# Performance work log

Hardware: AMD Instinct MI355X
Metric: run time of the kernel (lower is better)

Reference implementation:

```python
import jax, jax.numpy as jnp
import numpy as np

B, T = 8, 4096
H, V, K = 512, 32000, 9


def setup_inputs() -> dict:
    key = jax.random.key(0)
    k1, k2, k3 = jax.random.split(key, 3)
    x = jax.random.randint(k1, (B, T), 0, V, dtype=jnp.int32)
    # conv1d weight [out_ch=H, in_ch=V, K], xavier-like scale
    scale = 1.0 / np.sqrt(V * K)
    W = jax.random.normal(k2, (H, V, K), dtype=jnp.float32) * scale
    b = jax.random.normal(k3, (H,), dtype=jnp.float32) * 0.01
    return {"x": x, "W": W, "b": b}


def reference(x, W, b):
    """one_hot(x, V) -> conv1d(V->H, K, pad=K//2) expressed as gather+sum.

    out[b,t,c] = bias[c] + sum_k W[c, x[b, t+k-pad], k]  (zero outside [0,T)).
    """
    Bx, Tx = x.shape
    Hh, Vv, Kk = W.shape
    pad = Kk // 2
    t = jnp.arange(Tx)
    acc = jnp.zeros((Bx, Tx, Hh), dtype=W.dtype)
    for k in range(Kk):  # small fixed kernel loop (K=9)
        src = t + (k - pad)                      # [T]
        valid = (src >= 0) & (src < Tx)          # [T]
        src_c = jnp.clip(src, 0, Tx - 1)
        ids = x[:, src_c]                        # [B,T]
        emb = jnp.take(W[:, :, k].T, ids, axis=0)  # [B,T,H] gather of column k
        acc = acc + jnp.where(valid[None, :, None], emb, jnp.zeros((), W.dtype))
    return acc + b  # [B,T,H]
```

## Files before the change

kernel.cpp:

```cpp
#include <hip/hip_runtime.h>
#include <hip/hip_bf16.h>


#define Hc 512
#define Vc 32000
#define Kc 9
#define Tc 4096
#define Bc 8
#define Mc (Vc * Kc)
#define CHUNK_C 128
#define NCHUNK 4
#define ROW_U (Kc * CHUNK_C / 2)
#define WT_ROWS (Vc + 1)
#define T_TILE 32
#define NTB 9000
#define NGB 1024

__device__ __forceinline__ unsigned short f2bf(float f) {
  unsigned int u = __float_as_uint(f);
  u += 0x7FFFu + ((u >> 16) & 1u);
  return (unsigned short)(u >> 16);
}

__global__ __launch_bounds__(256) void mark_kernel(
    const int* __restrict__ x, int* __restrict__ slot, int* __restrict__ counter) {
  const int i = blockIdx.x * 256 + threadIdx.x;
  const int v = x[i];
  if (atomicCAS(&slot[v], -1, -2147483647) == -1) {
    slot[v] = 1 + atomicAdd(counter, 1);
  }
}

__global__ __launch_bounds__(256) void fused_kernel(
    const float* __restrict__ W, const int* __restrict__ x,
    const int* __restrict__ slot, const float* __restrict__ bias,
    float* __restrict__ out, unsigned int* __restrict__ wbuf,
    const unsigned int* __restrict__ rbuf, int tchunk, int gchunk) {
  __shared__ float tile[64][65];
  const int bx = blockIdx.x;
  const int rem = bx % 10;
  const int tid = threadIdx.x;

  if (rem != 9) {
    if (tchunk >= NCHUNK) return;
    const int tb = (bx / 10) * 9 + rem;
    if (tb >= NTB) return;
    const int mt = tb % 4500;
    const int ct = tb / 4500;
    const int m0 = mt * 64;
    const int cbase = tchunk * CHUNK_C + ct * 64;
    const int tx = tid & 63;
    const int ty = tid >> 6;
#pragma unroll
    for (int r = 0; r < 16; ++r) {
      const int row = ty * 16 + r;
      tile[row][tx] = W[(size_t)(cbase + row) * Mc + (m0 + tx)];
    }
    __syncthreads();
    const int u = tid & 31;
    const int rl = tid >> 5;
#pragma unroll
    for (int p = 0; p < 8; ++p) {
      const int mrow = p * 8 + rl;
      const int m = m0 + mrow;
      const int v = m / Kc;
      const int k = m - v * Kc;
      const int s = slot[v];
      if (s >= 0) {
        const unsigned int val =
            (unsigned int)f2bf(tile[2 * u][mrow]) |
            ((unsigned int)f2bf(tile[2 * u + 1][mrow]) << 16);
        wbuf[(size_t)s * ROW_U + k * (CHUNK_C / 2) + ct * 32 + u] = val;
      }
    }
  } else {
    if (gchunk < 0) return;
    const int gb = bx / 10;
    int* ids = (int*)tile;
    const int b = gb >> 7;
    const int t0 = (gb & 127) * T_TILE;
    if (tid < T_TILE + Kc - 1) {
      const int s = t0 + tid - (Kc / 2);
      ids[tid] = (s >= 0 && s < Tc) ? slot[x[b * Tc + s]] : 0;
    }
    __syncthreads();
    const int lane = tid & 63;
    const int w = tid >> 6;
    const int c0 = gchunk * CHUNK_C;
    const int cpair = c0 + 2 * lane;
    const float2 b2 = *(const float2*)(bias + cpair);
#pragma unroll
    for (int i = 0; i < 8; ++i) {
      const int tt = w * 8 + i;
      float2 acc = b2;
#pragma unroll
      for (int k = 0; k < Kc; ++k) {
        const int id = ids[tt + k];
        const unsigned int wv = rbuf[(size_t)id * ROW_U + k * (CHUNK_C / 2) + lane];
        acc.x += __uint_as_float(wv << 16);
        acc.y += __uint_as_float(wv & 0xFFFF0000u);
      }
      *(float2*)(out + ((size_t)(b * Tc + t0 + tt) << 9) + cpair) = acc;
    }
  }
}

__global__ __launch_bounds__(256) void conv_fallback_kernel(
    const int* __restrict__ x, const float* __restrict__ W,
    const float* __restrict__ bias, float* __restrict__ out) {
  const size_t idx = (size_t)blockIdx.x * 256 + threadIdx.x;
  const int c = (int)(idx & (Hc - 1));
  const size_t bt = idx >> 9;
  const int t = (int)(bt & (Tc - 1));
  const int b = (int)(bt >> 12);
  float acc = bias[c];
#pragma unroll
  for (int k = 0; k < Kc; ++k) {
    const int s = t + k - (Kc / 2);
    if (s >= 0 && s < Tc) {
      const int id = x[b * Tc + s];
      acc += W[(size_t)c * Mc + (size_t)id * Kc + k];
    }
  }
  out[idx] = acc;
}

extern "C" void kernel_launch(void* const* d_in, const int* in_sizes, int n_in,
                              void* d_out, int out_size, void* d_ws, size_t ws_size,
                              hipStream_t stream) {
  const int* x = (const int*)d_in[0];
  const float* W = (const float*)d_in[1];
  const float* bias = (const float*)d_in[2];
  float* out = (float*)d_out;

  const size_t buf_bytes = (size_t)WT_ROWS * ROW_U * 4;
  const size_t buf1_off = buf_bytes;
  const size_t slot_off = 2 * buf_bytes;
  const size_t cnt_off = slot_off + (size_t)Vc * 4;
  const size_t need = cnt_off + 4;

  if (ws_size >= need) {
    unsigned int* buf0 = (unsigned int*)d_ws;
    unsigned int* buf1 = (unsigned int*)((char*)d_ws + buf1_off);
    int* slot = (int*)((char*)d_ws + slot_off);
    int* counter = (int*)((char*)d_ws + cnt_off);
    hipMemsetAsync(slot, 0xFF, (size_t)Vc * 4, stream);
    hipMemsetAsync(counter, 0, 4, stream);
    hipMemsetAsync(buf0, 0, ROW_U * 4, stream);
    hipMemsetAsync(buf1, 0, ROW_U * 4, stream);
    mark_kernel<<<(Bc * Tc) / 256, 256, 0, stream>>>(x, slot, counter);
    const int grid = 10240;
    for (int l = 0; l <= NCHUNK; ++l) {
      const int tchunk = l;
      const int gchunk = l - 1;
      unsigned int* wbuf = (tchunk & 1) ? buf1 : buf0;
      const unsigned int* rbuf = (gchunk >= 0 && (gchunk & 1)) ? buf1 : buf0;
      fused_kernel<<<grid, 256, 0, stream>>>(W, x, slot, bias, out, wbuf, rbuf,
                                             tchunk, gchunk);
    }
  } else {
    const size_t n = (size_t)Bc * Tc * Hc;
    conv_fallback_kernel<<<(int)(n / 256), 256, 0, stream>>>(x, W, bias, out);
  }
}
```

Before: 244.4 us.

## Retile W transpose by vocab groups with swizzled LDS and vectorized bf16 writes

The transpose blocks now cover 7 whole vocab entries (63 m-columns) across all 128 channels of a chunk, where each previously covered 64 m-columns by 64 channels. Tiles go into a swizzled LDS buffer and are written out as uint2 rows per used vocab entry, and a whole vocab row is skipped when it never appears in the input. The grid shrinks to a 4:1 transpose-to-gather block ratio, and W loads and output stores become nontemporal. This aims to cut the per-element slot lookups and scattered 4-byte writes. In exchange, one of 64 lanes sits idle during loads and the per-vocab loop is serial within each block.

```diff
diff --git a/kernel.cpp b/kernel.cpp
--- a/kernel.cpp
+++ b/kernel.cpp
@@ -1,5 +1,6 @@
 #include <hip/hip_runtime.h>
 #include <hip/hip_bf16.h>
+#include <string.h>
 
 
 #define Hc 512
@@ -8,18 +9,21 @@
 #define Tc 4096
 #define Bc 8
 #define Mc (Vc * Kc)
+#define VT 7
+#define NMT 4572
+#define NM_TILE (VT * Kc)
 #define CHUNK_C 128
 #define NCHUNK 4
 #define ROW_U (Kc * CHUNK_C / 2)
 #define WT_ROWS (Vc + 1)
 #define T_TILE 32
-#define NTB 9000
 #define NGB 1024
+#define GRID_N 5715
 
-__device__ __forceinline__ unsigned short f2bf(float f) {
+__device__ __forceinline__ unsigned int f2bf(float f) {
   unsigned int u = __float_as_uint(f);
   u += 0x7FFFu + ((u >> 16) & 1u);
-  return (unsigned short)(u >> 16);
+  return u >> 16;
 }
 
 __global__ __launch_bounds__(256) void mark_kernel(
@@ -36,49 +40,17 @@
     const int* __restrict__ slot, const float* __restrict__ bias,
     float* __restrict__ out, unsigned int* __restrict__ wbuf,
     const unsigned int* __restrict__ rbuf, int tchunk, int gchunk) {
-  __shared__ float tile[64][65];
+  __shared__ float tile[NM_TILE * CHUNK_C];
   const int bx = blockIdx.x;
-  const int rem = bx % 10;
+  const int grp = bx / 5;
+  const int rem = bx % 5;
   const int tid = threadIdx.x;
 
-  if (rem != 9) {
-    if (tchunk >= NCHUNK) return;
-    const int tb = (bx / 10) * 9 + rem;
-    if (tb >= NTB) return;
-    const int mt = tb % 4500;
-    const int ct = tb / 4500;
-    const int m0 = mt * 64;
-    const int cbase = tchunk * CHUNK_C + ct * 64;
-    const int tx = tid & 63;
-    const int ty = tid >> 6;
-#pragma unroll
-    for (int r = 0; r < 16; ++r) {
-      const int row = ty * 16 + r;
-      tile[row][tx] = W[(size_t)(cbase + row) * Mc + (m0 + tx)];
-    }
-    __syncthreads();
-    const int u = tid & 31;
-    const int rl = tid >> 5;
-#pragma unroll
-    for (int p = 0; p < 8; ++p) {
-      const int mrow = p * 8 + rl;
-      const int m = m0 + mrow;
-      const int v = m / Kc;
-      const int k = m - v * Kc;
-      const int s = slot[v];
-      if (s >= 0) {
-        const unsigned int val =
-            (unsigned int)f2bf(tile[2 * u][mrow]) |
-            ((unsigned int)f2bf(tile[2 * u + 1][mrow]) << 16);
-        wbuf[(size_t)s * ROW_U + k * (CHUNK_C / 2) + ct * 32 + u] = val;
-      }
-    }
-  } else {
-    if (gchunk < 0) return;
-    const int gb = bx / 10;
+  if (rem == 4) {
+    if (gchunk < 0 || grp >= NGB) return;
     int* ids = (int*)tile;
-    const int b = gb >> 7;
-    const int t0 = (gb & 127) * T_TILE;
+    const int b = grp >> 7;
+    const int t0 = (grp & 127) * T_TILE;
     if (tid < T_TILE + Kc - 1) {
       const int s = t0 + tid - (Kc / 2);
       ids[tid] = (s >= 0 && s < Tc) ? slot[x[b * Tc + s]] : 0;
@@ -87,8 +59,8 @@
     const int lane = tid & 63;
     const int w = tid >> 6;
     const int c0 = gchunk * CHUNK_C;
-    const int cpair = c0 + 2 * lane;
-    const float2 b2 = *(const float2*)(bias + cpair);
+    const int cpl = 2 * lane;
+    const float2 b2 = *(const float2*)(bias + c0 + cpl);
 #pragma unroll
     for (int i = 0; i < 8; ++i) {
       const int tt = w * 8 + i;
@@ -96,11 +68,53 @@
 #pragma unroll
       for (int k = 0; k < Kc; ++k) {
         const int id = ids[tt + k];
-        const unsigned int wv = rbuf[(size_t)id * ROW_U + k * (CHUNK_C / 2) + lane];
+        const unsigned int wv =
+            rbuf[(size_t)id * ROW_U + k * (CHUNK_C / 2) + lane];
         acc.x += __uint_as_float(wv << 16);
         acc.y += __uint_as_float(wv & 0xFFFF0000u);
       }
-      *(float2*)(out + ((size_t)(b * Tc + t0 + tt) << 9) + cpair) = acc;
+      double d;
+      memcpy(&d, &acc, 8);
+      __builtin_nontemporal_store(
+          d, (double*)(out + ((size_t)(b * Tc + t0 + tt) << 9) + c0 + cpl));
+    }
+    return;
+  }
+
+  if (tchunk >= NCHUNK) return;
+  const int tb = grp * 4 + rem;
+  if (tb >= NMT) return;
+  const int v0 = tb * VT;
+  const int nv = (Vc - v0 < VT) ? (Vc - v0) : VT;
+  const int nm = nv * Kc;
+  const int m0 = v0 * Kc;
+  const int cbase = tchunk * CHUNK_C;
+  const int tx = tid & 63;
+  const int ty = tid >> 6;
+  if (tx < nm) {
+    const float* wp = W + (size_t)(cbase + ty * 32) * Mc + m0 + tx;
+#pragma unroll
+    for (int r = 0; r < 32; ++r) {
+      const int c = ty * 32 + r;
+      const float val = __builtin_nontemporal_load(wp + (size_t)r * Mc);
+      tile[tx * CHUNK_C + (c ^ ((tx & 7) << 2))] = val;
+    }
+  }
+  __syncthreads();
+  uint2* wbuf2 = (uint2*)wbuf;
+  for (int vl = 0; vl < nv; ++vl) {
+    const int s = slot[v0 + vl];
+    if (s < 0) continue;
+    for (int j = tid; j < 288; j += 256) {
+      const int k = j >> 5;
+      const int q = j & 31;
+      const int m = vl * Kc + k;
+      const float4 f =
+          *(const float4*)&tile[m * CHUNK_C + ((4 * q) ^ ((m & 7) << 2))];
+      uint2 val;
+      val.x = f2bf(f.x) | (f2bf(f.y) << 16);
+      val.y = f2bf(f.z) | (f2bf(f.w) << 16);
+      wbuf2[(size_t)s * 288 + j] = val;
     }
   }
 }
@@ -149,14 +163,13 @@
     hipMemsetAsync(buf0, 0, ROW_U * 4, stream);
     hipMemsetAsync(buf1, 0, ROW_U * 4, stream);
     mark_kernel<<<(Bc * Tc) / 256, 256, 0, stream>>>(x, slot, counter);
-    const int grid = 10240;
     for (int l = 0; l <= NCHUNK; ++l) {
       const int tchunk = l;
       const int gchunk = l - 1;
       unsigned int* wbuf = (tchunk & 1) ? buf1 : buf0;
       const unsigned int* rbuf = (gchunk >= 0 && (gchunk & 1)) ? buf1 : buf0;
-      fused_kernel<<<grid, 256, 0, stream>>>(W, x, slot, bias, out, wbuf, rbuf,
-                                             tchunk, gchunk);
+      fused_kernel<<<GRID_N, 256, 0, stream>>>(W, x, slot, bias, out, wbuf,
+                                               rbuf, tchunk, gchunk);
     }
   } else {
     const size_t n = (size_t)Bc * Tc * Hc;
```

Measured after the change: 254.7 us. 1.04x slower.

## Split fused transpose/gather pipeline into separate per-chunk kernels with single buffer

Applied to the files above, without the earlier changes.

Replaces the software-pipelined fused kernel, which overlapped the transpose of chunk l with the gather of chunk l-1 inside one grid using double buffers, with two separate kernels launched back to back per chunk over a single buffer. This removes the block-role dispatch and idle blocks from the interleaved grid and halves workspace use. The cost is losing overlap between the transpose and gather phases and adding more kernel launches.

```diff
diff --git a/kernel.cpp b/kernel.cpp
--- a/kernel.cpp
+++ b/kernel.cpp
@@ -13,13 +13,11 @@
 #define ROW_U (Kc * CHUNK_C / 2)
 #define WT_ROWS (Vc + 1)
 #define T_TILE 32
-#define NTB 9000
-#define NGB 1024
 
-__device__ __forceinline__ unsigned short f2bf(float f) {
+__device__ __forceinline__ unsigned int f2bf(float f) {
   unsigned int u = __float_as_uint(f);
   u += 0x7FFFu + ((u >> 16) & 1u);
-  return (unsigned short)(u >> 16);
+  return u >> 16;
 }
 
 __global__ __launch_bounds__(256) void mark_kernel(
@@ -31,77 +29,71 @@
   }
 }
 
-__global__ __launch_bounds__(256) void fused_kernel(
-    const float* __restrict__ W, const int* __restrict__ x,
-    const int* __restrict__ slot, const float* __restrict__ bias,
-    float* __restrict__ out, unsigned int* __restrict__ wbuf,
-    const unsigned int* __restrict__ rbuf, int tchunk, int gchunk) {
+__global__ __launch_bounds__(256) void transpose_chunk_kernel(
+    const float* __restrict__ W, const int* __restrict__ slot,
+    unsigned int* __restrict__ wbuf, int chunk) {
   __shared__ float tile[64][65];
-  const int bx = blockIdx.x;
-  const int rem = bx % 10;
+  const int m0 = blockIdx.x * 64;
+  const int ct = blockIdx.y;
+  const int cbase = chunk * CHUNK_C + ct * 64;
   const int tid = threadIdx.x;
+  const int tx = tid & 63;
+  const int ty = tid >> 6;
+#pragma unroll
+  for (int r = 0; r < 16; ++r) {
+    const int row = ty * 16 + r;
+    tile[row][tx] = W[(size_t)(cbase + row) * Mc + (m0 + tx)];
+  }
+  __syncthreads();
+  const int u = tid & 31;
+  const int rl = tid >> 5;
+#pragma unroll
+  for (int p = 0; p < 8; ++p) {
+    const int mrow = p * 8 + rl;
+    const int m = m0 + mrow;
+    const int v = m / Kc;
+    const int k = m - v * Kc;
+    const int s = slot[v];
+    if (s >= 0) {
+      const unsigned int val = f2bf(tile[2 * u][mrow]) |
+                               (f2bf(tile[2 * u + 1][mrow]) << 16);
+      wbuf[(size_t)s * ROW_U + k * (CHUNK_C / 2) + ct * 32 + u] = val;
+    }
+  }
+}
 
-  if (rem != 9) {
-    if (tchunk >= NCHUNK) return;
-    const int tb = (bx / 10) * 9 + rem;
-    if (tb >= NTB) return;
-    const int mt = tb % 4500;
-    const int ct = tb / 4500;
-    const int m0 = mt * 64;
-    const int cbase = tchunk * CHUNK_C + ct * 64;
-    const int tx = tid & 63;
-    const int ty = tid >> 6;
+__global__ __launch_bounds__(256) void gather_chunk_kernel(
+    const int* __restrict__ x, const int* __restrict__ slot,
+    const unsigned int* __restrict__ rbuf, const float* __restrict__ bias,
+    float* __restrict__ out, int chunk) {
+  __shared__ int ids[T_TILE + Kc - 1];
+  const int gb = blockIdx.x;
+  const int b = gb >> 7;
+  const int t0 = (gb & 127) * T_TILE;
+  const int tid = threadIdx.x;
+  if (tid < T_TILE + Kc - 1) {
+    const int s = t0 + tid - (Kc / 2);
+    ids[tid] = (s >= 0 && s < Tc) ? slot[x[b * Tc + s]] : 0;
+  }
+  __syncthreads();
+  const int lane = tid & 63;
+  const int w = tid >> 6;
+  const int c0 = chunk * CHUNK_C;
+  const int cpl = 2 * lane;
+  const float2 b2 = *(const float2*)(bias + c0 + cpl);
 #pragma unroll
-    for (int r = 0; r < 16; ++r) {
-      const int row = ty * 16 + r;
-      tile[row][tx] = W[(size_t)(cbase + row) * Mc + (m0 + tx)];
+  for (int i = 0; i < 8; ++i) {
+    const int tt = w * 8 + i;
+    float2 acc = b2;
+#pragma unroll
+    for (int k = 0; k < Kc; ++k) {
+      const int id = ids[tt + k];
+      const unsigned int wv =
+          rbuf[(size_t)id * ROW_U + k * (CHUNK_C / 2) + lane];
+      acc.x += __uint_as_float(wv << 16);
+      acc.y += __uint_as_float(wv & 0xFFFF0000u);
     }
-    __syncthreads();
-    const int u = tid & 31;
-    const int rl = tid >> 5;
-#pragma unroll
-    for (int p = 0; p < 8; ++p) {
-      const int mrow = p * 8 + rl;
-      const int m = m0 + mrow;
-      const int v = m / Kc;
-      const int k = m - v * Kc;
-      const int s = slot[v];
-      if (s >= 0) {
-        const unsigned int val =
-            (unsigned int)f2bf(tile[2 * u][mrow]) |
-            ((unsigned int)f2bf(tile[2 * u + 1][mrow]) << 16);
-        wbuf[(size_t)s * ROW_U + k * (CHUNK_C / 2) + ct * 32 + u] = val;
-      }
-    }
-  } else {
-    if (gchunk < 0) return;
-    const int gb = bx / 10;
-    int* ids = (int*)tile;
-    const int b = gb >> 7;
-    const int t0 = (gb & 127) * T_TILE;
-    if (tid < T_TILE + Kc - 1) {
-      const int s = t0 + tid - (Kc / 2);
-      ids[tid] = (s >= 0 && s < Tc) ? slot[x[b * Tc + s]] : 0;
-    }
-    __syncthreads();
-    const int lane = tid & 63;
-    const int w = tid >> 6;
-    const int c0 = gchunk * CHUNK_C;
-    const int cpair = c0 + 2 * lane;
-    const float2 b2 = *(const float2*)(bias + cpair);
-#pragma unroll
-    for (int i = 0; i < 8; ++i) {
-      const int tt = w * 8 + i;
-      float2 acc = b2;
-#pragma unroll
-      for (int k = 0; k < Kc; ++k) {
-        const int id = ids[tt + k];
-        const unsigned int wv = rbuf[(size_t)id * ROW_U + k * (CHUNK_C / 2) + lane];
-        acc.x += __uint_as_float(wv << 16);
-        acc.y += __uint_as_float(wv & 0xFFFF0000u);
-      }
-      *(float2*)(out + ((size_t)(b * Tc + t0 + tt) << 9) + cpair) = acc;
-    }
+    *(float2*)(out + ((size_t)(b * Tc + t0 + tt) << 9) + c0 + cpl) = acc;
   }
 }
 
@@ -134,29 +126,23 @@
   float* out = (float*)d_out;
 
   const size_t buf_bytes = (size_t)WT_ROWS * ROW_U * 4;
-  const size_t buf1_off = buf_bytes;
-  const size_t slot_off = 2 * buf_bytes;
+  const size_t slot_off = buf_bytes;
   const size_t cnt_off = slot_off + (size_t)Vc * 4;
   const size_t need = cnt_off + 4;
 
   if (ws_size >= need) {
-    unsigned int* buf0 = (unsigned int*)d_ws;
-    unsigned int* buf1 = (unsigned int*)((char*)d_ws + buf1_off);
+    unsigned int* buf = (unsigned int*)d_ws;
     int* slot = (int*)((char*)d_ws + slot_off);
     int* counter = (int*)((char*)d_ws + cnt_off);
     hipMemsetAsync(slot, 0xFF, (size_t)Vc * 4, stream);
     hipMemsetAsync(counter, 0, 4, stream);
-    hipMemsetAsync(buf0, 0, ROW_U * 4, stream);
-    hipMemsetAsync(buf1, 0, ROW_U * 4, stream);
+    hipMemsetAsync(buf, 0, ROW_U * 4, stream);
     mark_kernel<<<(Bc * Tc) / 256, 256, 0, stream>>>(x, slot, counter);
-    const int grid = 10240;
-    for (int l = 0; l <= NCHUNK; ++l) {
-      const int tchunk = l;
-      const int gchunk = l - 1;
-      unsigned int* wbuf = (tchunk & 1) ? buf1 : buf0;
-      const unsigned int* rbuf = (gchunk >= 0 && (gchunk & 1)) ? buf1 : buf0;
-      fused_kernel<<<grid, 256, 0, stream>>>(W, x, slot, bias, out, wbuf, rbuf,
-                                             tchunk, gchunk);
+    dim3 tg(4500, 2);
+    for (int chunk = 0; chunk < NCHUNK; ++chunk) {
+      transpose_chunk_kernel<<<tg, 256, 0, stream>>>(W, slot, buf, chunk);
+      gather_chunk_kernel<<<1024, 256, 0, stream>>>(x, slot, buf, bias, out,
+                                                    chunk);
     }
   } else {
     const size_t n = (size_t)Bc * Tc * Hc;
```

Result: no change. 241.0 us (-1.4%).
